# Kernel tuning notes

Hardware: AMD Instinct MI355X
Metric: run time of the kernel (lower is better)

Reference implementation:

```python
import jax, jax.numpy as jnp
import numpy as np

Tx, Ty, Bn = 48, 48, 64
DW, E, D, A = 512, 512, 1024, 512   # dim_wemb, dim_enc, dim_dec, dim_att
VS, VT = 32000, 32000


def setup_inputs() -> dict:
    key = jax.random.key(0)
    ks = iter(jax.random.split(key, 40))
    def p(shape, s=0.05):
        return jax.random.normal(next(ks), shape, jnp.float32) * s
    inp = {
        "x_data": jax.random.randint(next(ks), (Tx, Bn), 0, VS),
        "x_mask": jnp.ones((Tx, Bn), jnp.float32),
        "y_data": jax.random.randint(next(ks), (Ty, Bn), 0, VT),
        "y_mask": jnp.ones((Ty, Bn), jnp.float32),
        "src_emb": p((VS, DW)),
        "dec_emb": p((VT, DW)),
        # encoder bidirectional LSTM (gate order i,f,g,o; b = b_ih + b_hh)
        "enc_Wih_f": p((4 * E, DW)), "enc_Whh_f": p((4 * E, E)), "enc_b_f": jnp.zeros((4 * E,), jnp.float32),
        "enc_Wih_r": p((4 * E, DW)), "enc_Whh_r": p((4 * E, E)), "enc_b_r": jnp.zeros((4 * E,), jnp.float32),
        "h0_W": p((D, 2 * E)), "h0_b": jnp.zeros((D,), jnp.float32),
        "c0_W": p((D, 2 * E)), "c0_b": jnp.zeros((D,), jnp.float32),
        "att1_W": p((A, 2 * E + DW + D)), "att1_b": jnp.zeros((A,), jnp.float32),
        "att2_W": p((1, A)), "att2_b": jnp.zeros((1,), jnp.float32),
        "cell_Wih": p((4 * D, DW + 2 * E)), "cell_Whh": p((4 * D, D)), "cell_b": jnp.zeros((4 * D,), jnp.float32),
        "read_W": p((2 * DW, 2 * E + D + DW)), "read_b": jnp.zeros((2 * DW,), jnp.float32),
        "out_W": p((VT, DW)), "out_b": jnp.zeros((VT,), jnp.float32),
    }
    return inp


def _lstm(x_seq, Wih, Whh, b, reverse):
    # x_seq: [T, B, in]; returns hidden states [T, B, H] (PyTorch LSTM equations)
    B = x_seq.shape[1]
    H = Whh.shape[1]
    def step(carry, x_t):
        h, c = carry
        z = x_t @ Wih.T + h @ Whh.T + b
        i, f, g, o = jnp.split(z, 4, axis=-1)
        c = jax.nn.sigmoid(f) * c + jax.nn.sigmoid(i) * jnp.tanh(g)
        h = jax.nn.sigmoid(o) * jnp.tanh(c)
        return (h, c), h
    init = (jnp.zeros((B, H), x_seq.dtype), jnp.zeros((B, H), x_seq.dtype))
    _, ys = jax.lax.scan(step, init, x_seq, reverse=reverse)
    return ys


def reference(x_data, x_mask, y_data, y_mask, src_emb, dec_emb,
              enc_Wih_f, enc_Whh_f, enc_b_f, enc_Wih_r, enc_Whh_r, enc_b_r,
              h0_W, h0_b, c0_W, c0_b, att1_W, att1_b, att2_W, att2_b,
              cell_Wih, cell_Whh, cell_b, read_W, read_b, out_W, out_b):
    B = x_data.shape[1]
    # ---- encoder ----
    x_emb = src_emb[x_data] * x_mask[..., None]                       # [Tx,B,DW]
    out_f = _lstm(x_emb, enc_Wih_f, enc_Whh_f, enc_b_f, reverse=False)
    out_r = _lstm(x_emb, enc_Wih_r, enc_Whh_r, enc_b_r, reverse=True)
    ctx = jnp.concatenate([out_f, out_r], axis=-1) * x_mask[..., None]  # [Tx,B,2E]
    # ---- decoder init ----
    ctx_mean = (ctx * x_mask[..., None]).sum(0) / x_mask.sum(0)[:, None]
    ht = jnp.tanh(ctx_mean @ h0_W.T + h0_b)
    ct = jnp.tanh(ctx_mean @ c0_W.T + c0_b)
    # split additive-attention weight: ctx part precomputed once (same math as concat)
    W1c = att1_W[:, : 2 * E]
    W1y = att1_W[:, 2 * E: 2 * E + DW]
    W1h = att1_W[:, 2 * E + DW:]
    att_ctx = jnp.einsum('tbe,ae->tba', ctx, W1c) + att1_b            # [Tx,B,A]
    # teacher forcing: y_prev[0] = 0 (like the zero-initialized yt), then y_data shifted
    y_prev = jnp.concatenate([jnp.zeros((1, B), y_data.dtype), y_data[:-1]], axis=0)

    def step(carry, xs):
        ht, ct = carry
        yp, yt, ym = xs
        y_emb = dec_emb[yp]                                           # [B,DW]
        a1 = jnp.tanh(att_ctx + y_emb @ W1y.T + ht @ W1h.T)           # [Tx,B,A]
        a2 = (a1 @ att2_W.T + att2_b)[..., 0]                         # [Tx,B]
        a2 = a2 - jnp.max(a2)                                         # global max, as in torch.max(att2)
        alpha = jnp.exp(a2) * x_mask
        alpha = alpha / (alpha.sum(0, keepdims=True) + 1e-15)
        ctx_t = (alpha[..., None] * ctx).sum(0)                       # [B,2E]
        dec_in = jnp.concatenate([y_emb, ctx_t], axis=1)
        z = dec_in @ cell_Wih.T + ht @ cell_Whh.T + cell_b
        i, f, g, o = jnp.split(z, 4, axis=-1)
        ct = jax.nn.sigmoid(f) * ct + jax.nn.sigmoid(i) * jnp.tanh(g)
        ht = jax.nn.sigmoid(o) * jnp.tanh(ct)
        readin = jnp.concatenate([ctx_t, ht, y_emb], axis=1)
        r = (readin @ read_W.T + read_b).reshape(B, DW, 2).max(-1)    # maxout pairs
        logp = jax.nn.log_softmax(r @ out_W.T + out_b, axis=-1)       # [B,VT]
        nll = -jnp.take_along_axis(logp, yt[:, None], axis=1)[:, 0]
        loss_t = (nll * ym).sum() / B
        return (ht, ct), loss_t

    _, losses = jax.lax.scan(step, (ht, ct), (y_prev, y_data, y_mask))
    return losses.sum()
```

## Files before the change

### kernel.cpp

```cpp
#include <hip/hip_runtime.h>
#include <hip/hip_bf16.h>
#include <math.h>

typedef __attribute__((ext_vector_type(8))) short bf16x8;
typedef __attribute__((ext_vector_type(4))) short bf16x4;
typedef __attribute__((ext_vector_type(4))) float f32x4;
typedef unsigned short u16;
typedef unsigned int u32;

__device__ __forceinline__ float bf2f(u16 u) {
    union { float f; u32 i; } v; v.i = ((u32)u) << 16; return v.f;
}
__device__ __forceinline__ float bflo(u32 v) {
    union { float f; u32 u; } x; x.u = v << 16; return x.f;
}
__device__ __forceinline__ float bfhi(u32 v) {
    union { float f; u32 u; } x; x.u = v & 0xFFFF0000u; return x.f;
}
__device__ __forceinline__ u16 f2bf(float x) {
    union { float f; u32 u; } v; v.f = x;
    u32 r = v.u + 0x7FFF + ((v.u >> 16) & 1);
    return (u16)(r >> 16);
}
__device__ __forceinline__ u32 f2bf2(float a, float b) {
    return (u32)f2bf(a) | ((u32)f2bf(b) << 16);
}
__device__ __forceinline__ float sigf(float x) { return 1.0f / (1.0f + expf(-x)); }

__device__ __forceinline__ void st_wt_u16(u16* p, u16 v) {
    asm volatile("global_store_short %0, %1, off sc0 sc1" :: "v"(p), "v"((u32)v) : "memory");
}
__device__ __forceinline__ void st_wt_f32(float* p, float v) {
    asm volatile("global_store_dword %0, %1, off sc0 sc1" :: "v"(p), "v"(v) : "memory");
}
__device__ __forceinline__ void st_wt_u32(u32* p, u32 v) {
    asm volatile("global_store_dword %0, %1, off sc0 sc1" :: "v"(p), "v"(v) : "memory");
}

__device__ __forceinline__ void gbarH(u32* flags, u32* go, int myidx, int aggbid,
                                      u32 ph, int nblk, int nrepmask) {
    __syncthreads();
    if ((int)blockIdx.x == aggbid) {
        if (threadIdx.x == 0) st_wt_u32(flags + (size_t)myidx * 16, ph);
        if (threadIdx.x < 64) {
            bool ok = false;
            if (nblk == 256) {
                const u32* p = flags + (size_t)threadIdx.x * 64;
                while (!ok) {
                    u32 a, b, c, d;
                    asm volatile(
                        "global_load_dword %0, %4, off sc0 sc1\n\t"
                        "global_load_dword %1, %5, off sc0 sc1\n\t"
                        "global_load_dword %2, %6, off sc0 sc1\n\t"
                        "global_load_dword %3, %7, off sc0 sc1\n\t"
                        "s_waitcnt vmcnt(0)"
                        : "=&v"(a), "=&v"(b), "=&v"(c), "=&v"(d)
                        : "v"(p), "v"(p + 16), "v"(p + 32), "v"(p + 48)
                        : "memory");
                    ok = __all((a >= ph) && (b >= ph) && (c >= ph) && (d >= ph));
                }
            } else {
                const u32* p = flags + (size_t)threadIdx.x * 16;
                while (!ok) {
                    u32 a;
                    asm volatile("global_load_dword %0, %1, off sc0 sc1\n\ts_waitcnt vmcnt(0)"
                                 : "=&v"(a) : "v"(p) : "memory");
                    ok = __all(a >= ph);
                }
            }
            if ((int)threadIdx.x <= nrepmask)
                st_wt_u32(go + (size_t)threadIdx.x * 16, ph);
        }
        __syncthreads();
    } else {
        if (threadIdx.x == 0) {
            st_wt_u32(flags + (size_t)myidx * 16, ph);
            const u32* gp = go + (size_t)(myidx & nrepmask) * 16;
            u32 v;
            do {
                asm volatile("global_load_dword %0, %1, off sc0 sc1\n\ts_waitcnt vmcnt(0)"
                             : "=&v"(v) : "v"(gp) : "memory");
            } while (v < ph);
        }
        __syncthreads();
    }
}

template<int OUTBF, int ACT, int CIN>
__global__ __launch_bounds__(256) void mgemm(
    const u16* __restrict__ A, int lda,
    const u16* __restrict__ B, int ldb,
    const float* __restrict__ bias,
    const u16* __restrict__ Cin,
    void* __restrict__ Cout,
    int N, int K,
    const u16* A2, const u16* B2, const float* bias2, const u16* Cin2, void* Cout2)
{
    if (blockIdx.z == 1) { A = A2; B = B2; bias = bias2; Cin = Cin2; Cout = Cout2; }
    const int lane = threadIdx.x & 63;
    const int wave = threadIdx.x >> 6;
    const int wm = wave >> 1, wn = wave & 1;
    const int lr = lane & 15, lg = lane >> 4;
    const size_t bm = (size_t)blockIdx.y * 64, bn = (size_t)blockIdx.x * 64;
    const u16* Ap = A + (bm + wm * 32 + lr) * (size_t)lda + lg * 8;
    const u16* Bp = B + (bn + wn * 32 + lr) * (size_t)ldb + lg * 8;
    f32x4 acc[2][2] = {};
    for (int k0 = 0; k0 < K; k0 += 32) {
        bf16x8 a0 = *(const bf16x8*)(Ap + k0);
        bf16x8 a1 = *(const bf16x8*)(Ap + k0 + 16 * (size_t)lda);
        bf16x8 b0 = *(const bf16x8*)(Bp + k0);
        bf16x8 b1 = *(const bf16x8*)(Bp + k0 + 16 * (size_t)ldb);
        acc[0][0] = __builtin_amdgcn_mfma_f32_16x16x32_bf16(a0, b0, acc[0][0], 0, 0, 0);
        acc[0][1] = __builtin_amdgcn_mfma_f32_16x16x32_bf16(a0, b1, acc[0][1], 0, 0, 0);
        acc[1][0] = __builtin_amdgcn_mfma_f32_16x16x32_bf16(a1, b0, acc[1][0], 0, 0, 0);
        acc[1][1] = __builtin_amdgcn_mfma_f32_16x16x32_bf16(a1, b1, acc[1][1], 0, 0, 0);
    }
    #pragma unroll
    for (int fi = 0; fi < 2; ++fi)
    #pragma unroll
    for (int fj = 0; fj < 2; ++fj) {
        size_t col = bn + wn * 32 + fj * 16 + lr;
        float bv = bias ? bias[col] : 0.0f;
        #pragma unroll
        for (int r = 0; r < 4; ++r) {
            size_t row = bm + wm * 32 + fi * 16 + lg * 4 + r;
            float v = acc[fi][fj][r] + bv;
            if constexpr (CIN) v += bf2f(Cin[row * (size_t)N + col]);
            if constexpr (ACT) v = tanhf(v);
            if constexpr (OUTBF) ((u16*)Cout)[row * (size_t)N + col] = f2bf(v);
            else                 ((float*)Cout)[row * (size_t)N + col] = v;
        }
    }
}

__global__ __launch_bounds__(256, 1) void enc_persist(
    const u16* __restrict__ WhhFg, const u16* __restrict__ WhhRg,
    const u16* __restrict__ preAF, const u16* __restrict__ preAR,
    const float* __restrict__ bF, const float* __restrict__ bR,
    const float* __restrict__ xm,
    u16* hAbuf, u16* hBbuf,
    u16* __restrict__ ctxB, u32* encSync)
{
    const int tid = threadIdx.x, bid = blockIdx.x;
    const int lane = tid & 63, wave = tid >> 6;
    const int lr = lane & 15, lg = lane >> 4;
    const int dir = bid >> 6;
    const int nb = bid & 63;
    const u16* Whh = dir ? WhhRg : WhhFg;
    const u16* preA = dir ? preAR : preAF;
    const float* bias = dir ? bR : bF;
    u16* hbase = dir ? hBbuf : hAbuf;
    u32* flags = encSync + (size_t)dir * 1280;
    u32* go = flags + 1024;
    const int aggbid = dir * 64;
    __shared__ u16 whh[32 * 520];
    __shared__ float zs[64 * 33];
    for (int i = tid; i < 32 * 64; i += 256) {
        int r = i >> 6, c = (i & 63) * 8;
        *(bf16x8*)&whh[r * 520 + c] = *(const bf16x8*)&Whh[(size_t)(nb * 32 + r) * 512 + c];
    }
    __syncthreads();
    const int gb = tid & 63, dl0 = tid >> 6;
    float creg[2] = {0.f, 0.f};
    u32 ph = 0;
    for (int s = 0; s < 48; ++s) {
        const int t = dir ? (47 - s) : s;
        if (s > 0) {
            const u16* hc = hbase + (size_t)s * 32768;
            const u16* Ap = hc + (wave * 16 + lr) * 512 + lg * 8;
            f32x4 acc0 = {}, acc1 = {};
            #pragma unroll 4
            for (int k0 = 0; k0 < 512; k0 += 32) {
                bf16x8 a  = *(const bf16x8*)(Ap + k0);
                bf16x8 b0 = *(const bf16x8*)&whh[lr * 520 + k0 + lg * 8];
                bf16x8 b1 = *(const bf16x8*)&whh[(16 + lr) * 520 + k0 + lg * 8];
                acc0 = __builtin_amdgcn_mfma_f32_16x16x32_bf16(a, b0, acc0, 0, 0, 0);
                acc1 = __builtin_amdgcn_mfma_f32_16x16x32_bf16(a, b1, acc1, 0, 0, 0);
            }
            #pragma unroll
            for (int r = 0; r < 4; ++r) {
                int row = wave * 16 + lg * 4 + r;
                zs[row * 33 + lr] = acc0[r];
                zs[row * 33 + 16 + lr] = acc1[r];
            }
            __syncthreads();
        }
        u16* hnx = hbase + (size_t)(s + 1) * 32768;
        #pragma unroll
        for (int q = 0; q < 2; ++q) {
            int dl = dl0 + q * 4;
            int dg = nb * 8 + dl;
            bf16x4 pa = *(const bf16x4*)&preA[((size_t)t * 64 + gb) * 2048 + nb * 32 + 4 * dl];
            float iv = bf2f((u16)pa[0]) + bias[dg];
            float fv = bf2f((u16)pa[1]) + bias[512 + dg];
            float gv = bf2f((u16)pa[2]) + bias[1024 + dg];
            float ov = bf2f((u16)pa[3]) + bias[1536 + dg];
            if (s > 0) {
                iv += zs[gb * 33 + 4 * dl + 0];
                fv += zs[gb * 33 + 4 * dl + 1];
                gv += zs[gb * 33 + 4 * dl + 2];
                ov += zs[gb * 33 + 4 * dl + 3];
            }
            float cn = sigf(fv) * creg[q] + sigf(iv) * tanhf(gv);
            float hn = sigf(ov) * tanhf(cn);
            creg[q] = cn;
            st_wt_u16(&hnx[gb * 512 + dg], f2bf(hn));
            ctxB[((size_t)t * 64 + gb) * 1024 + dir * 512 + dg] = f2bf(hn * xm[t * 64 + gb]);
        }
        if (s < 47) gbarH(flags, go, nb, aggbid, ++ph, 64, 15);
    }
}

__global__ __launch_bounds__(512, 1) void dec_persist(
    const u16* __restrict__ WzB, const u16* __restrict__ W1hB,
    const u16* __restrict__ attctxB, const u16* __restrict__ ctxB,
    const u16* __restrict__ preYB, const u16* __restrict__ yembB,
    const float* __restrict__ att2W, const float* __restrict__ att2b,
    const float* __restrict__ xmask, const float* __restrict__ cellb,
    u16* htR, const float* __restrict__ ctF,
    float* svB, float* zpartR, const u16* __restrict__ G,
    u16* c3r, u32* decFlags, u32* decGo)
{
    const int tid = threadIdx.x, bid = blockIdx.x;
    const int lane = tid & 63, wave = tid >> 6;
    const int lr = lane & 15, lg = lane >> 4;
    const int b = bid >> 2;
    const int q = bid & 3;
    const int cb = ((bid & 7) << 5) | (bid >> 3);
    __shared__ u16 big[48 * 512];
    __shared__ u16 wzl[16 * 1544];
    __shared__ u16 w1h[2 * 1024];
    __shared__ float scr[8352];
    __shared__ float a2s[64];

    for (int i = tid; i < 48 * 64; i += 512) {
        int tp = i >> 6, c = (i & 63) * 8;
        *(bf16x8*)&big[tp * 512 + c] =
            *(const bf16x8*)&attctxB[((size_t)tp * 64 + b) * 512 + c];
    }
    for (int i = tid; i < 16 * 192; i += 512) {
        int r = i / 192, c = (i % 192) * 8;
        *(bf16x8*)&wzl[r * 1544 + c] =
            *(const bf16x8*)&WzB[(size_t)(cb * 16 + r) * 2560 + 1024 + c];
    }
    for (int i = tid; i < 256; i += 512) {
        int r = i >> 7, c = (i & 127) * 8;
        *(bf16x8*)&w1h[r * 1024 + c] = *(const bf16x8*)&W1hB[(size_t)(bid * 2 + r) * 1024 + c];
    }
    float a2wreg[8];
    #pragma unroll
    for (int k = 0; k < 8; ++k) a2wreg[k] = att2W[k * 64 + lane];
    float xmr = (tid < 64) ? xmask[tid * 64 + b] : 0.f;
    const int n0 = q * 1024 + 2 * tid;
    u32 gfrag[48];
    #pragma unroll
    for (int tp = 0; tp < 48; ++tp)
        gfrag[tp] = *(const u32*)&G[((size_t)tp * 64 + b) * 4096 + n0];
    const int d = n0 >> 2;
    const int glo = (tid & 1) ? 2 : 0;
    const float cb0 = cellb[glo * 1024 + d];
    const float cb1 = cellb[(glo + 1) * 1024 + d];
    float ct_reg = (tid & 1) ? 0.f : ctF[b * 1024 + d];
    __syncthreads();
    const float att2b0 = att2b[0];

    auto svz_phase = [&](int tt) {
        const u16* htT = htR + (size_t)tt * 65536;
        if (wave < 4) {
            const int jl = wave & 1;
            const int bh = wave >> 1;
            const int j = bid * 2 + jl;
            float* svT = svB + (size_t)tt * 32768;
            bf16x8 wv0 = *(const bf16x8*)&w1h[jl * 1024 + lane * 8];
            bf16x8 wv1 = *(const bf16x8*)&w1h[jl * 1024 + 512 + lane * 8];
            float s[32];
            #pragma unroll 8
            for (int bi = 0; bi < 32; ++bi) {
                const u16* hp = htT + (bh * 32 + bi) * 1024 + lane * 8;
                bf16x8 h0 = *(const bf16x8*)(hp);
                bf16x8 h1 = *(const bf16x8*)(hp + 512);
                float a = 0.f;
                #pragma unroll
                for (int u = 0; u < 8; ++u)
                    a += bf2f((u16)h0[u]) * bf2f((u16)wv0[u])
                       + bf2f((u16)h1[u]) * bf2f((u16)wv1[u]);
                s[bi] = a;
            }
            float* zone = scr + wave * 2080;
            #pragma unroll 8
            for (int bi = 0; bi < 32; ++bi) zone[bi * 65 + lane] = s[bi];
            if (lane < 32) {
                const float* zr = zone + lane * 65;
                float tsum = 0.f;
                #pragma unroll
                for (int u = 0; u < 64; ++u) tsum += zr[u];
                int bb = bh * 32 + lane;
                st_wt_f32(&svT[bb * 512 + j],
                          tsum + bf2f(preYB[((size_t)tt * 64 + bb) * 512 + j]));
            }
        } else {
            const int bt = wave - 4;
            const u16* Ah = htT + (bt * 16 + lr) * 1024 + lg * 8;
            const u16* Ay = yembB + ((size_t)tt * 64 + bt * 16 + lr) * 512 + lg * 8;
            const u16* Bp = &wzl[lr * 1544 + lg * 8];
            f32x4 acc = {};
            #pragma unroll 4
            for (int k0 = 0; k0 < 1024; k0 += 32) {
                bf16x8 a = *(const bf16x8*)(Ah + k0);
                bf16x8 bw = *(const bf16x8*)(Bp + k0);
                acc = __builtin_amdgcn_mfma_f32_16x16x32_bf16(a, bw, acc, 0, 0, 0);
            }
            #pragma unroll 4
            for (int k0 = 0; k0 < 512; k0 += 32) {
                bf16x8 a = *(const bf16x8*)(Ay + k0);
                bf16x8 bw = *(const bf16x8*)(Bp + 1024 + k0);
                acc = __builtin_amdgcn_mfma_f32_16x16x32_bf16(a, bw, acc, 0, 0, 0);
            }
            float* zpT = zpartR + (size_t)tt * 262144;
            #pragma unroll
            for (int r = 0; r < 4; ++r) {
                int bb = bt * 16 + lg * 4 + r;
                st_wt_f32(&zpT[(size_t)bb * 4096 + cb * 16 + lr], acc[r]);
            }
        }
    };

    u32 ph = 0;
    svz_phase(0);
    gbarH(decFlags, decGo, bid, 255, ++ph, 256, 31);

    for (int t = 0; t < 48; ++t) {
        {
            const float* svT = svB + (size_t)t * 32768;
            float svr[8];
            #pragma unroll
            for (int k = 0; k < 8; ++k) svr[k] = svT[b * 512 + k * 64 + lane];
            for (int tp = wave; tp < 48; tp += 8) {
                float s = 0.f;
                #pragma unroll
                for (int k = 0; k < 8; ++k)
                    s += a2wreg[k] * tanhf(bf2f(big[tp * 512 + k * 64 + lane]) + svr[k]);
                #pragma unroll
                for (int m = 32; m; m >>= 1) s += __shfl_xor(s, m);
                if (lane == 0) a2s[tp] = s + att2b0;
            }
            __syncthreads();
            if (tid < 64) {
                float v = (tid < 48) ? a2s[tid] : -1e30f;
                float m = v;
                #pragma unroll
                for (int sh = 32; sh; sh >>= 1) m = fmaxf(m, __shfl_xor(m, sh));
                float e = (tid < 48) ? expf(v - m) * xmr : 0.f;
                float ssum = e;
                #pragma unroll
                for (int sh = 32; sh; sh >>= 1) ssum += __shfl_xor(ssum, sh);
                if (tid < 48) a2s[tid] = e / (ssum + 1e-15f);
            }
            __syncthreads();
            float2 zp2 = *(const float2*)&zpartR[(size_t)t * 262144 + (size_t)b * 4096 + n0];
            float z0 = cb0 + zp2.x, z1 = cb1 + zp2.y;
            #pragma unroll
            for (int tp = 0; tp < 48; ++tp) {
                float al = a2s[tp];
                u32 g = gfrag[tp];
                z0 += al * bflo(g); z1 += al * bfhi(g);
            }
            {
                int gg = tid >> 7, cp = tid & 127;
                float c0 = 0.f, c1 = 0.f;
                #pragma unroll
                for (int u = 0; u < 12; ++u) {
                    int tp = gg * 12 + u;
                    float al = a2s[tp];
                    u32 cv = *(const u32*)&ctxB[((size_t)tp * 64 + b) * 1024 + q * 256 + 2 * cp];
                    c0 += al * bflo(cv); c1 += al * bfhi(cv);
                }
                scr[(gg * 128 + cp) * 2]     = c0;
                scr[(gg * 128 + cp) * 2 + 1] = c1;
            }
            __syncthreads();
            u16* c3rt = c3r + (size_t)t * 64 * 2560 + (size_t)b * 2560;
            if (tid < 128) {
                float c0 = scr[tid * 2]     + scr[(128 + tid) * 2]
                         + scr[(256 + tid) * 2] + scr[(384 + tid) * 2];
                float c1 = scr[tid * 2 + 1]     + scr[(128 + tid) * 2 + 1]
                         + scr[(256 + tid) * 2 + 1] + scr[(384 + tid) * 2 + 1];
                *(u32*)&c3rt[q * 256 + 2 * tid] = f2bf2(c0, c1);
            } else if (tid < 192) {
                int i = tid - 128;
                *(u32*)&c3rt[2048 + q * 128 + 2 * i] =
                    *(const u32*)&yembB[((size_t)t * 64 + b) * 512 + q * 128 + 2 * i];
            }
            float zg = __shfl_xor(z0, 1);
            float zo = __shfl_xor(z1, 1);
            if (!(tid & 1)) {
                float cn = sigf(z1) * ct_reg + sigf(z0) * tanhf(zg);
                float hn = sigf(zo) * tanhf(cn);
                ct_reg = cn;
                u16 hb = f2bf(hn);
                st_wt_u16(&htR[(size_t)(t + 1) * 65536 + b * 1024 + d], hb);
                c3rt[1024 + d] = hb;
            }
        }
        if (t < 47) {
            gbarH(decFlags, decGo, bid, 255, ++ph, 256, 31);
            svz_phase(t + 1);
            gbarH(decFlags, decGo, bid, 255, ++ph, 256, 31);
        }
    }
}

__global__ __launch_bounds__(256) void logits_lsm(
    const u16* __restrict__ A, const u16* __restrict__ B,
    const float* __restrict__ outb, const int* __restrict__ ydata,
    float2* __restrict__ part, float* __restrict__ logy)
{
    const int lane = threadIdx.x & 63;
    const int wave = threadIdx.x >> 6;
    const int wm = wave >> 1, wn = wave & 1;
    const int lr = lane & 15, lg = lane >> 4;
    const size_t bm = (size_t)blockIdx.x * 64, bn = (size_t)blockIdx.y * 64;
    const u16* Ap = A + (bm + wm * 32 + lr) * 512 + lg * 8;
    const u16* Bp = B + (bn + wn * 32 + lr) * 512 + lg * 8;
    f32x4 acc[2][2] = {};
    for (int k0 = 0; k0 < 512; k0 += 32) {
        bf16x8 a0 = *(const bf16x8*)(Ap + k0);
        bf16x8 a1 = *(const bf16x8*)(Ap + k0 + 16 * 512);
        bf16x8 b0 = *(const bf16x8*)(Bp + k0);
        bf16x8 b1 = *(const bf16x8*)(Bp + k0 + 16 * 512);
        acc[0][0] = __builtin_amdgcn_mfma_f32_16x16x32_bf16(a0, b0, acc[0][0], 0, 0, 0);
        acc[0][1] = __builtin_amdgcn_mfma_f32_16x16x32_bf16(a0, b1, acc[0][1], 0, 0, 0);
        acc[1][0] = __builtin_amdgcn_mfma_f32_16x16x32_bf16(a1, b0, acc[1][0], 0, 0, 0);
        acc[1][1] = __builtin_amdgcn_mfma_f32_16x16x32_bf16(a1, b1, acc[1][1], 0, 0, 0);
    }
    __shared__ float sm[64][2];
    __shared__ float ss[64][2];
    const float b0 = outb[bn + wn * 32 + lr];
    const float b1 = outb[bn + wn * 32 + 16 + lr];
    #pragma unroll
    for (int fi = 0; fi < 2; ++fi) {
        #pragma unroll
        for (int r = 0; r < 4; ++r) {
            int rloc = wm * 32 + fi * 16 + lg * 4 + r;
            size_t row = bm + rloc;
            float v0 = acc[fi][0][r] + b0;
            float v1 = acc[fi][1][r] + b1;
            int yt = ydata[row];
            if (yt == (int)(bn + wn * 32 + lr))      logy[row] = v0;
            if (yt == (int)(bn + wn * 32 + 16 + lr)) logy[row] = v1;
            float m = fmaxf(v0, v1);
            #pragma unroll
            for (int sh = 1; sh < 16; sh <<= 1) m = fmaxf(m, __shfl_xor(m, sh));
            float s = expf(v0 - m) + expf(v1 - m);
            #pragma unroll
            for (int sh = 1; sh < 16; sh <<= 1) s += __shfl_xor(s, sh);
            if (lr == 0) { sm[rloc][wn] = m; ss[rloc][wn] = s; }
        }
    }
    __syncthreads();
    if (threadIdx.x < 64) {
        float m0 = sm[threadIdx.x][0], m1 = sm[threadIdx.x][1];
        float m = fmaxf(m0, m1);
        float s = ss[threadIdx.x][0] * expf(m0 - m) + ss[threadIdx.x][1] * expf(m1 - m);
        part[(bm + threadIdx.x) * 500 + blockIdx.y] = make_float2(m, s);
    }
}

__global__ __launch_bounds__(64) void lsm_reduce(
    const float2* __restrict__ part, const float* __restrict__ logy,
    const float* __restrict__ ymask, float* __restrict__ lossb)
{
    int r = blockIdx.x, lane = threadIdx.x;
    float m = -1e30f;
    for (int i = lane; i < 500; i += 64) m = fmaxf(m, part[(size_t)r * 500 + i].x);
    #pragma unroll
    for (int sh = 32; sh; sh >>= 1) m = fmaxf(m, __shfl_xor(m, sh));
    float s = 0.f;
    for (int i = lane; i < 500; i += 64) {
        float2 p = part[(size_t)r * 500 + i];
        s += p.y * expf(p.x - m);
    }
    #pragma unroll
    for (int sh = 32; sh; sh >>= 1) s += __shfl_xor(s, sh);
    if (lane == 0) {
        float lp = logy[r] - m - logf(s);
        lossb[r] = -lp * ymask[r] * (1.0f / 64.0f);
    }
}

__global__ void convb(const float* __restrict__ src, int sld, int K,
                      u16* __restrict__ dst, int total)
{
    int idx = blockIdx.x * 256 + threadIdx.x;
    if (idx >= total) return;
    int n = idx / K, k = idx - n * K;
    dst[idx] = f2bf(src[(size_t)n * sld + k]);
}

__global__ void conv_gate4(const float* __restrict__ src, u16* __restrict__ dst,
                           int H, int K, int total)
{
    int idx = blockIdx.x * 256 + threadIdx.x;
    if (idx >= total) return;
    int n = idx / K, k = idx - n * K;
    int d = n >> 2, g = n & 3;
    dst[idx] = f2bf(src[(size_t)(g * H + d) * K + k]);
}

__global__ void build_wz_g4(const float* __restrict__ Wih, const float* __restrict__ Whh,
                            u16* __restrict__ Wz)
{
    int idx = blockIdx.x * 256 + threadIdx.x;
    int j = idx % 2560, np = idx / 2560;
    int n = (np & 3) * 1024 + (np >> 2);
    float v;
    if (j < 1024)      v = Wih[(size_t)n * 1536 + 512 + j];
    else if (j < 2048) v = Whh[(size_t)n * 1024 + (j - 1024)];
    else               v = Wih[(size_t)n * 1536 + (j - 2048)];
    Wz[idx] = f2bf(v);
}

__global__ void embed_kernel(const int* __restrict__ xd, const float* __restrict__ xm,
                             const int* __restrict__ yd,
                             const float* __restrict__ src_emb, const float* __restrict__ dec_emb,
                             u16* __restrict__ x_emb, u16* __restrict__ y_emb)
{
    int idx = blockIdx.x * 256 + threadIdx.x;
    int d = idx & 511;
    int tb = idx >> 9;
    if (blockIdx.y == 0) {
        int v = xd[tb];
        x_emb[idx] = f2bf(src_emb[(size_t)v * 512 + d] * xm[tb]);
    } else {
        int t = tb >> 6, b = tb & 63;
        int v = (t == 0) ? 0 : yd[(t - 1) * 64 + b];
        y_emb[idx] = f2bf(dec_emb[(size_t)v * 512 + d]);
    }
}

__global__ __launch_bounds__(256) void ctx_mean_k(const u16* __restrict__ ctxB,
                                                  const float* __restrict__ xm,
                                                  u16* __restrict__ cm)
{
    int b = blockIdx.x, tid = threadIdx.x;
    float msum = 0.f;
    for (int t = 0; t < 48; ++t) msum += xm[t * 64 + b];
    float inv = 1.0f / msum;
    for (int e = tid; e < 1024; e += 256) {
        float s = 0.f;
        for (int t = 0; t < 48; ++t)
            s += bf2f(ctxB[(size_t)(t * 64 + b) * 1024 + e]) * xm[t * 64 + b];
        cm[b * 1024 + e] = f2bf(s * inv);
    }
}

__global__ void maxpair(const u16* __restrict__ rB, u16* __restrict__ rmax)
{
    int idx = blockIdx.x * 256 + threadIdx.x;
    int row = idx >> 9, d = idx & 511;
    float a = bf2f(rB[(size_t)row * 1024 + 2 * d]);
    float b = bf2f(rB[(size_t)row * 1024 + 2 * d + 1]);
    rmax[idx] = f2bf(fmaxf(a, b));
}

__global__ __launch_bounds__(256) void final_sum(const float* __restrict__ lossb,
                                                 float* __restrict__ out)
{
    __shared__ float red[4];
    int tid = threadIdx.x;
    float s = 0.f;
    for (int i = tid; i < 3072; i += 256) s += lossb[i];
    for (int sh = 32; sh; sh >>= 1) s += __shfl_xor(s, sh);
    if ((tid & 63) == 0) red[tid >> 6] = s;
    __syncthreads();
    if (tid == 0) out[0] = red[0] + red[1] + red[2] + red[3];
}

template<int OUTBF, int ACT, int CIN>
static void mg(hipStream_t st, dim3 grid,
               const u16* A, int lda, const u16* B, int ldb,
               const float* bias, const u16* Cin, void* C, int N, int K,
               const u16* A2 = nullptr, const u16* B2 = nullptr,
               const float* bias2 = nullptr, const u16* Cin2 = nullptr, void* C2 = nullptr)
{
    hipLaunchKernelGGL((mgemm<OUTBF, ACT, CIN>), grid, dim3(256), 0, st,
                       A, lda, B, ldb, bias, Cin, C, N, K, A2, B2, bias2, Cin2, C2);
}

extern "C" void kernel_launch(void* const* d_in, const int* in_sizes, int n_in,
                              void* d_out, int out_size, void* d_ws, size_t ws_size,
                              hipStream_t stream)
{
    const int*   x_data    = (const int*)d_in[0];
    const float* x_mask    = (const float*)d_in[1];
    const int*   y_data    = (const int*)d_in[2];
    const float* y_mask    = (const float*)d_in[3];
    const float* src_emb   = (const float*)d_in[4];
    const float* dec_emb   = (const float*)d_in[5];
    const float* enc_Wih_f = (const float*)d_in[6];
    const float* enc_Whh_f = (const float*)d_in[7];
    const float* enc_b_f   = (const float*)d_in[8];
    const float* enc_Wih_r = (const float*)d_in[9];
    const float* enc_Whh_r = (const float*)d_in[10];
    const float* enc_b_r   = (const float*)d_in[11];
    const float* h0_W      = (const float*)d_in[12];
    const float* h0_b      = (const float*)d_in[13];
    const float* c0_W      = (const float*)d_in[14];
    const float* c0_b      = (const float*)d_in[15];
    const float* att1_W    = (const float*)d_in[16];
    const float* att1_b    = (const float*)d_in[17];
    const float* att2_W    = (const float*)d_in[18];
    const float* att2_b    = (const float*)d_in[19];
    const float* cell_Wih  = (const float*)d_in[20];
    const float* cell_Whh  = (const float*)d_in[21];
    const float* cell_b    = (const float*)d_in[22];
    const float* read_W    = (const float*)d_in[23];
    const float* read_b    = (const float*)d_in[24];
    const float* out_W     = (const float*)d_in[25];
    const float* out_b     = (const float*)d_in[26];
    float* out = (float*)d_out;
    (void)in_sizes; (void)n_in; (void)out_size; (void)ws_size;

    char* base = (char*)d_ws;
    size_t off = 0;
    auto ab = [&](size_t bytes) -> void* {
        void* p = base + off;
        off += (bytes + 255) & ~(size_t)255;
        return p;
    };
    u16* WzB     = (u16*)ab(4096UL * 2560 * 2);
    u16* outWB   = (u16*)ab(32000UL * 512 * 2);
    u16* readWB  = (u16*)ab(1024UL * 2560 * 2);
    u16* WihFg   = (u16*)ab(2048UL * 512 * 2);
    u16* WihRg   = (u16*)ab(2048UL * 512 * 2);
    u16* WhhFg   = (u16*)ab(2048UL * 512 * 2);
    u16* WhhRg   = (u16*)ab(2048UL * 512 * 2);
    u16* h0WB    = (u16*)ab(1024UL * 1024 * 2);
    u16* c0WB    = (u16*)ab(1024UL * 1024 * 2);
    u16* W1cB    = (u16*)ab(512UL * 1024 * 2);
    u16* W1yB    = (u16*)ab(512UL * 512 * 2);
    u16* W1hB    = (u16*)ab(512UL * 1024 * 2);
    u16* xembB   = (u16*)ab(3072UL * 512 * 2);
    u16* yembB   = (u16*)ab(3072UL * 512 * 2);
    u16* preAF   = (u16*)ab(3072UL * 2048 * 2);
    u16* preAR   = (u16*)ab(3072UL * 2048 * 2);
    u16* G       = preAF;
    float2* part = (float2*)preAF;
    u16* rB      = (u16*)((char*)preAF + 12288000);
    u16* rmaxB   = (u16*)((char*)preAF + 12288000 + 6291456);
    u16* ctxB    = (u16*)ab(3072UL * 1024 * 2);
    u16* attctxB = (u16*)ab(3072UL * 512 * 2);
    u16* preYB   = (u16*)ab(3072UL * 512 * 2);
    u16* cmB     = (u16*)ab(64UL * 1024 * 2);
    u16* hAbuf   = (u16*)ab(49UL * 64 * 512 * 2);
    u16* hBbuf   = (u16*)ab(49UL * 64 * 512 * 2);
    u16* htR     = (u16*)ab(49UL * 64 * 1024 * 2);
    float* ctF   = (float*)ab(64UL * 1024 * 4);
    float* svB   = (float*)ab(48UL * 64 * 512 * 4);
    float* zpartR= (float*)ab(48UL * 64 * 4096 * 4);
    u16* c3r     = (u16*)ab(3072UL * 2560 * 2);
    float* logy  = (float*)ab(3072UL * 4);
    float* lossb = (float*)ab(3072UL * 4);
    u32* sync    = (u32*)ab(32768);
    u32* decFlags = sync;
    u32* decGo    = sync + 4096;
    u32* encSync  = sync + 4608;

    hipMemsetAsync(sync, 0, 32768, stream);
    hipMemsetAsync(hAbuf, 0, 64UL * 512 * 2, stream);
    hipMemsetAsync(hBbuf, 0, 64UL * 512 * 2, stream);
    hipLaunchKernelGGL(build_wz_g4, dim3(40960), dim3(256), 0, stream, cell_Wih, cell_Whh, WzB);
    auto conv = [&](const float* src, int sld, int K, u16* dst, size_t total) {
        hipLaunchKernelGGL(convb, dim3((unsigned)((total + 255) / 256)), dim3(256), 0, stream,
                           src, sld, K, dst, (int)total);
    };
    auto convg = [&](const float* src, u16* dst, int H, int K) {
        size_t total = (size_t)4 * H * K;
        hipLaunchKernelGGL(conv_gate4, dim3((unsigned)((total + 255) / 256)), dim3(256), 0, stream,
                           src, dst, H, K, (int)total);
    };
    conv(out_W, 512, 512, outWB, 32000UL * 512);
    conv(read_W, 2560, 2560, readWB, 1024UL * 2560);
    convg(enc_Wih_f, WihFg, 512, 512);
    convg(enc_Wih_r, WihRg, 512, 512);
    convg(enc_Whh_f, WhhFg, 512, 512);
    convg(enc_Whh_r, WhhRg, 512, 512);
    conv(h0_W, 1024, 1024, h0WB, 1024UL * 1024);
    conv(c0_W, 1024, 1024, c0WB, 1024UL * 1024);
    conv(att1_W, 2560, 1024, W1cB, 512UL * 1024);
    conv(att1_W + 1024, 2560, 512, W1yB, 512UL * 512);
    conv(att1_W + 1536, 2560, 1024, W1hB, 512UL * 1024);
    hipLaunchKernelGGL(embed_kernel, dim3(6144, 2), dim3(256), 0, stream,
                       x_data, x_mask, y_data, src_emb, dec_emb, xembB, yembB);

    mg<1, 0, 0>(stream, dim3(32, 48, 2), xembB, 512, WihFg, 512, nullptr, nullptr,
                preAF, 2048, 512, xembB, WihRg, nullptr, nullptr, preAR);

    hipLaunchKernelGGL(enc_persist, dim3(128), dim3(256), 0, stream,
                       WhhFg, WhhRg, preAF, preAR, enc_b_f, enc_b_r, x_mask,
                       hAbuf, hBbuf, ctxB, encSync);

    mg<1, 0, 0>(stream, dim3(64, 48, 1), ctxB, 1024, WzB, 2560, nullptr, nullptr,
                G, 4096, 1024);

    hipLaunchKernelGGL(ctx_mean_k, dim3(64), dim3(256), 0, stream, ctxB, x_mask, cmB);
    mg<1, 1, 0>(stream, dim3(16, 1, 1), cmB, 1024, h0WB, 1024, h0_b, nullptr, htR, 1024, 1024);
    mg<0, 1, 0>(stream, dim3(16, 1, 1), cmB, 1024, c0WB, 1024, c0_b, nullptr, ctF, 1024, 1024);
    mg<1, 0, 0>(stream, dim3(8, 48, 1), ctxB, 1024, W1cB, 1024, att1_b, nullptr, attctxB, 512, 1024);
    mg<1, 0, 0>(stream, dim3(8, 48, 1), yembB, 512, W1yB, 512, nullptr, nullptr, preYB, 512, 512);

    hipLaunchKernelGGL(dec_persist, dim3(256), dim3(512), 0, stream,
                       WzB, W1hB, attctxB, ctxB, preYB, yembB, att2_W, att2_b,
                       x_mask, cell_b, htR, ctF, svB, zpartR, G, c3r, decFlags, decGo);

    mg<1, 0, 0>(stream, dim3(16, 48, 1), c3r, 2560, readWB, 2560, read_b, nullptr, rB, 1024, 2560);
    hipLaunchKernelGGL(maxpair, dim3(6144), dim3(256), 0, stream, rB, rmaxB);
    hipLaunchKernelGGL(logits_lsm, dim3(48, 500), dim3(256), 0, stream,
                       rmaxB, outWB, out_b, y_data, part, logy);
    hipLaunchKernelGGL(lsm_reduce, dim3(3072), dim3(64), 0, stream, part, logy, y_mask, lossb);
    hipLaunchKernelGGL(final_sum, dim3(1), dim3(256), 0, stream, lossb, out);
}
```

Before: 2.770 ms.

## Fuse maxout into read GEMM, halve encoder blocks, hoist zpart load

Fuses the maxout pair reduction into the read-projection GEMM epilogue using a lane shuffle, which removes the separate maxpair kernel and the intermediate rB buffer round trip. The encoder persistent kernel now runs 64 blocks of 512 threads, each owning 64 gate rows instead of 32. This halves the number of participants in the per-step grid barrier, and the barrier poll was adjusted so only active lanes spin. In the decoder, the zpartR load is hoisted ahead of the attention softmax so its latency overlaps that work. The costs are more LDS per encoder block and fewer CUs in use during the recurrence.

```diff
diff --git a/kernel.cpp b/kernel.cpp
--- a/kernel.cpp
+++ b/kernel.cpp
@@ -43,8 +43,8 @@
     if ((int)blockIdx.x == aggbid) {
         if (threadIdx.x == 0) st_wt_u32(flags + (size_t)myidx * 16, ph);
         if (threadIdx.x < 64) {
-            bool ok = false;
             if (nblk == 256) {
+                bool ok = false;
                 const u32* p = flags + (size_t)threadIdx.x * 64;
                 while (!ok) {
                     u32 a, b, c, d;
@@ -61,11 +61,14 @@
                 }
             } else {
                 const u32* p = flags + (size_t)threadIdx.x * 16;
-                while (!ok) {
-                    u32 a;
-                    asm volatile("global_load_dword %0, %1, off sc0 sc1\n\ts_waitcnt vmcnt(0)"
-                                 : "=&v"(a) : "v"(p) : "memory");
-                    ok = __all(a >= ph);
+                bool okl = ((int)threadIdx.x >= nblk);
+                while (!__all(okl)) {
+                    if (!okl) {
+                        u32 a;
+                        asm volatile("global_load_dword %0, %1, off sc0 sc1\n\ts_waitcnt vmcnt(0)"
+                                     : "=&v"(a) : "v"(p) : "memory");
+                        okl = (a >= ph);
+                    }
                 }
             }
             if ((int)threadIdx.x <= nrepmask)
@@ -86,7 +89,7 @@
     }
 }
 
-template<int OUTBF, int ACT, int CIN>
+template<int OUTBF, int ACT, int CIN, int MAXP = 0>
 __global__ __launch_bounds__(256) void mgemm(
     const u16* __restrict__ A, int lda,
     const u16* __restrict__ B, int ldb,
@@ -127,13 +130,20 @@
             float v = acc[fi][fj][r] + bv;
             if constexpr (CIN) v += bf2f(Cin[row * (size_t)N + col]);
             if constexpr (ACT) v = tanhf(v);
-            if constexpr (OUTBF) ((u16*)Cout)[row * (size_t)N + col] = f2bf(v);
-            else                 ((float*)Cout)[row * (size_t)N + col] = v;
-        }
-    }
-}
-
-__global__ __launch_bounds__(256, 1) void enc_persist(
+            if constexpr (MAXP) {
+                float vmax = fmaxf(v, __shfl_xor(v, 1));
+                if (!(lane & 1))
+                    ((u16*)Cout)[row * (size_t)(N >> 1) + (col >> 1)] = f2bf(vmax);
+            } else if constexpr (OUTBF) {
+                ((u16*)Cout)[row * (size_t)N + col] = f2bf(v);
+            } else {
+                ((float*)Cout)[row * (size_t)N + col] = v;
+            }
+        }
+    }
+}
+
+__global__ __launch_bounds__(512, 1) void enc_persist(
     const u16* __restrict__ WhhFg, const u16* __restrict__ WhhRg,
     const u16* __restrict__ preAF, const u16* __restrict__ preAR,
     const float* __restrict__ bF, const float* __restrict__ bR,
@@ -144,62 +154,63 @@
     const int tid = threadIdx.x, bid = blockIdx.x;
     const int lane = tid & 63, wave = tid >> 6;
     const int lr = lane & 15, lg = lane >> 4;
-    const int dir = bid >> 6;
-    const int nb = bid & 63;
+    const int dir = bid >> 5;
+    const int nb = bid & 31;
     const u16* Whh = dir ? WhhRg : WhhFg;
     const u16* preA = dir ? preAR : preAF;
     const float* bias = dir ? bR : bF;
     u16* hbase = dir ? hBbuf : hAbuf;
     u32* flags = encSync + (size_t)dir * 1280;
     u32* go = flags + 1024;
-    const int aggbid = dir * 64;
-    __shared__ u16 whh[32 * 520];
-    __shared__ float zs[64 * 33];
-    for (int i = tid; i < 32 * 64; i += 256) {
+    const int aggbid = dir * 32;
+    __shared__ u16 whh[64 * 520];
+    __shared__ float zs[64 * 66];
+    for (int i = tid; i < 64 * 64; i += 512) {
         int r = i >> 6, c = (i & 63) * 8;
-        *(bf16x8*)&whh[r * 520 + c] = *(const bf16x8*)&Whh[(size_t)(nb * 32 + r) * 512 + c];
+        *(bf16x8*)&whh[r * 520 + c] = *(const bf16x8*)&Whh[(size_t)(nb * 64 + r) * 512 + c];
     }
     __syncthreads();
     const int gb = tid & 63, dl0 = tid >> 6;
+    const int wr = wave & 3, wc = wave >> 2;
     float creg[2] = {0.f, 0.f};
     u32 ph = 0;
     for (int s = 0; s < 48; ++s) {
         const int t = dir ? (47 - s) : s;
         if (s > 0) {
             const u16* hc = hbase + (size_t)s * 32768;
-            const u16* Ap = hc + (wave * 16 + lr) * 512 + lg * 8;
+            const u16* Ap = hc + (wr * 16 + lr) * 512 + lg * 8;
             f32x4 acc0 = {}, acc1 = {};
             #pragma unroll 4
             for (int k0 = 0; k0 < 512; k0 += 32) {
                 bf16x8 a  = *(const bf16x8*)(Ap + k0);
-                bf16x8 b0 = *(const bf16x8*)&whh[lr * 520 + k0 + lg * 8];
-                bf16x8 b1 = *(const bf16x8*)&whh[(16 + lr) * 520 + k0 + lg * 8];
+                bf16x8 b0 = *(const bf16x8*)&whh[(wc * 32 + lr) * 520 + k0 + lg * 8];
+                bf16x8 b1 = *(const bf16x8*)&whh[(wc * 32 + 16 + lr) * 520 + k0 + lg * 8];
                 acc0 = __builtin_amdgcn_mfma_f32_16x16x32_bf16(a, b0, acc0, 0, 0, 0);
                 acc1 = __builtin_amdgcn_mfma_f32_16x16x32_bf16(a, b1, acc1, 0, 0, 0);
             }
             #pragma unroll
             for (int r = 0; r < 4; ++r) {
-                int row = wave * 16 + lg * 4 + r;
-                zs[row * 33 + lr] = acc0[r];
-                zs[row * 33 + 16 + lr] = acc1[r];
+                int row = wr * 16 + lg * 4 + r;
+                zs[row * 66 + wc * 32 + lr] = acc0[r];
+                zs[row * 66 + wc * 32 + 16 + lr] = acc1[r];
             }
             __syncthreads();
         }
         u16* hnx = hbase + (size_t)(s + 1) * 32768;
         #pragma unroll
         for (int q = 0; q < 2; ++q) {
-            int dl = dl0 + q * 4;
-            int dg = nb * 8 + dl;
-            bf16x4 pa = *(const bf16x4*)&preA[((size_t)t * 64 + gb) * 2048 + nb * 32 + 4 * dl];
+            int dlocal = dl0 + 8 * q;
+            int dg = nb * 16 + dlocal;
+            bf16x4 pa = *(const bf16x4*)&preA[((size_t)t * 64 + gb) * 2048 + nb * 64 + 4 * dlocal];
             float iv = bf2f((u16)pa[0]) + bias[dg];
             float fv = bf2f((u16)pa[1]) + bias[512 + dg];
             float gv = bf2f((u16)pa[2]) + bias[1024 + dg];
             float ov = bf2f((u16)pa[3]) + bias[1536 + dg];
             if (s > 0) {
-                iv += zs[gb * 33 + 4 * dl + 0];
-                fv += zs[gb * 33 + 4 * dl + 1];
-                gv += zs[gb * 33 + 4 * dl + 2];
-                ov += zs[gb * 33 + 4 * dl + 3];
+                iv += zs[gb * 66 + 4 * dlocal + 0];
+                fv += zs[gb * 66 + 4 * dlocal + 1];
+                gv += zs[gb * 66 + 4 * dlocal + 2];
+                ov += zs[gb * 66 + 4 * dlocal + 3];
             }
             float cn = sigf(fv) * creg[q] + sigf(iv) * tanhf(gv);
             float hn = sigf(ov) * tanhf(cn);
@@ -207,7 +218,7 @@
             st_wt_u16(&hnx[gb * 512 + dg], f2bf(hn));
             ctxB[((size_t)t * 64 + gb) * 1024 + dir * 512 + dg] = f2bf(hn * xm[t * 64 + gb]);
         }
-        if (s < 47) gbarH(flags, go, nb, aggbid, ++ph, 64, 15);
+        if (s < 47) gbarH(flags, go, nb, aggbid, ++ph, 32, 7);
     }
 }
 
@@ -331,6 +342,7 @@
 
     for (int t = 0; t < 48; ++t) {
         {
+            float2 zp2 = *(const float2*)&zpartR[(size_t)t * 262144 + (size_t)b * 4096 + n0];
             const float* svT = svB + (size_t)t * 32768;
             float svr[8];
             #pragma unroll
@@ -357,7 +369,6 @@
                 if (tid < 48) a2s[tid] = e / (ssum + 1e-15f);
             }
             __syncthreads();
-            float2 zp2 = *(const float2*)&zpartR[(size_t)t * 262144 + (size_t)b * 4096 + n0];
             float z0 = cb0 + zp2.x, z1 = cb1 + zp2.y;
             #pragma unroll
             for (int tp = 0; tp < 48; ++tp) {
@@ -554,15 +565,6 @@
     }
 }
 
-__global__ void maxpair(const u16* __restrict__ rB, u16* __restrict__ rmax)
-{
-    int idx = blockIdx.x * 256 + threadIdx.x;
-    int row = idx >> 9, d = idx & 511;
-    float a = bf2f(rB[(size_t)row * 1024 + 2 * d]);
-    float b = bf2f(rB[(size_t)row * 1024 + 2 * d + 1]);
-    rmax[idx] = f2bf(fmaxf(a, b));
-}
-
 __global__ __launch_bounds__(256) void final_sum(const float* __restrict__ lossb,
                                                  float* __restrict__ out)
 {
@@ -576,14 +578,14 @@
     if (tid == 0) out[0] = red[0] + red[1] + red[2] + red[3];
 }
 
-template<int OUTBF, int ACT, int CIN>
+template<int OUTBF, int ACT, int CIN, int MAXP = 0>
 static void mg(hipStream_t st, dim3 grid,
                const u16* A, int lda, const u16* B, int ldb,
                const float* bias, const u16* Cin, void* C, int N, int K,
                const u16* A2 = nullptr, const u16* B2 = nullptr,
                const float* bias2 = nullptr, const u16* Cin2 = nullptr, void* C2 = nullptr)
 {
-    hipLaunchKernelGGL((mgemm<OUTBF, ACT, CIN>), grid, dim3(256), 0, st,
+    hipLaunchKernelGGL((mgemm<OUTBF, ACT, CIN, MAXP>), grid, dim3(256), 0, st,
                        A, lda, B, ldb, bias, Cin, C, N, K, A2, B2, bias2, Cin2, C2);
 }
 
@@ -646,8 +648,7 @@
     u16* preAR   = (u16*)ab(3072UL * 2048 * 2);
     u16* G       = preAF;
     float2* part = (float2*)preAF;
-    u16* rB      = (u16*)((char*)preAF + 12288000);
-    u16* rmaxB   = (u16*)((char*)preAF + 12288000 + 6291456);
+    u16* rmaxB   = (u16*)((char*)preAF + 12288000);
     u16* ctxB    = (u16*)ab(3072UL * 1024 * 2);
     u16* attctxB = (u16*)ab(3072UL * 512 * 2);
     u16* preYB   = (u16*)ab(3072UL * 512 * 2);
@@ -696,7 +697,7 @@
     mg<1, 0, 0>(stream, dim3(32, 48, 2), xembB, 512, WihFg, 512, nullptr, nullptr,
                 preAF, 2048, 512, xembB, WihRg, nullptr, nullptr, preAR);
 
-    hipLaunchKernelGGL(enc_persist, dim3(128), dim3(256), 0, stream,
+    hipLaunchKernelGGL(enc_persist, dim3(64), dim3(512), 0, stream,
                        WhhFg, WhhRg, preAF, preAR, enc_b_f, enc_b_r, x_mask,
                        hAbuf, hBbuf, ctxB, encSync);
 
@@ -713,8 +714,8 @@
                        WzB, W1hB, attctxB, ctxB, preYB, yembB, att2_W, att2_b,
                        x_mask, cell_b, htR, ctF, svB, zpartR, G, c3r, decFlags, decGo);
 
-    mg<1, 0, 0>(stream, dim3(16, 48, 1), c3r, 2560, readWB, 2560, read_b, nullptr, rB, 1024, 2560);
-    hipLaunchKernelGGL(maxpair, dim3(6144), dim3(256), 0, stream, rB, rmaxB);
+    mg<1, 0, 0, 1>(stream, dim3(16, 48, 1), c3r, 2560, readWB, 2560, read_b, nullptr,
+                   rmaxB, 1024, 2560);
     hipLaunchKernelGGL(logits_lsm, dim3(48, 500), dim3(256), 0, stream,
                        rmaxB, outWB, out_b, y_data, part, logy);
     hipLaunchKernelGGL(lsm_reduce, dim3(3072), dim3(64), 0, stream, part, logy, y_mask, lossb);
```

New measurement: 2.904 ms. 4.8% more time.
